# Kernel optimization log

Measured on AMD Instinct MI355X. Metric: run time of the kernel, lower is better.

The kernel has to match this reference:

```python
import jax, jax.numpy as jnp
import numpy as np

B, C_IN, IMG, PATCH = 16, 3, 512, 16
C_FEAT, N_CLS, K = 2048, 18, 24  # K cells per image (fixed -> jit-friendly ragged groups)
HF = IMG // PATCH  # 32
N_CELLS = B * K
EPS = 1e-6


def setup_inputs() -> dict:
    key = jax.random.key(0)
    ks = jax.random.split(key, 8)
    return {
        "cell_img": jax.random.normal(ks[0], (B, C_IN, IMG, IMG), jnp.float32),
        "cell_masks": jax.random.uniform(ks[1], (N_CELLS, HF, HF), jnp.float32),
        "cell_counts": jnp.full((B,), K, dtype=jnp.int32),
        "W_backbone": jax.random.normal(ks[2], (C_FEAT, C_IN, PATCH, PATCH), jnp.float32) * 0.02,
        "b_backbone": jnp.zeros((C_FEAT,), jnp.float32),
        "W_final": jax.random.normal(ks[3], (N_CLS, C_FEAT, 1, 1), jnp.float32) * 0.02,
        "b_final": jnp.zeros((N_CLS,), jnp.float32),
        "W1": jax.random.normal(ks[4], (1024, C_FEAT), jnp.float32) * 0.02,
        "b1": jnp.zeros((1024,), jnp.float32),
        "W2": jax.random.normal(ks[5], (N_CLS, 1024), jnp.float32) * 0.02,
        "b2": jnp.zeros((N_CLS,), jnp.float32),
    }


def _forward(cell_img, cell_masks, cell_counts, W_backbone, b_backbone,
             W_final, b_final, W1, b1, W2, b2):
    # backbone: patch-embed style conv, 3 -> 2048, stride 16 -> [B, 2048, 32, 32]
    fm = jax.lax.conv_general_dilated(
        cell_img, W_backbone, (PATCH, PATCH), "VALID",
        dimension_numbers=("NCHW", "OIHW", "NCHW"))
    fm = jax.nn.relu(fm + b_backbone[None, :, None, None])
    # final_conv: 1x1 conv 2048 -> 18 class maps
    class_maps = jnp.einsum("bchw,oc->bohw", fm, W_final[:, :, 0, 0]) + b_final[None, :, None, None]

    # masked-RoI average pooling (feature_roi / class_roi)
    fm2 = fm.reshape(B, C_FEAT, HF * HF)            # [B, C, P]
    cm2 = class_maps.reshape(B, N_CLS, HF * HF)     # [B, 18, P]
    masksB = cell_masks.reshape(B, K, HF * HF)      # [B, K, P]
    area = masksB.sum(-1, keepdims=True) + EPS       # [B, K, 1]
    cell_features = jnp.einsum("bkp,bcp->bkc", masksB, fm2) / area   # [B, K, 2048]
    cell_class_logits = jnp.einsum("bkp,bcp->bkc", masksB, cm2) / area  # [B, K, 18]

    # fc_cell_weights (Dropout is identity at eval)
    h = jax.nn.relu(jnp.einsum("bkc,oc->bko", cell_features, W1) + b1)
    cell_weight_logits = jnp.einsum("bkh,oh->bko", h, W2) + b2       # [B, K, 18]

    # per-image (segment) softmax over cells + attention-weighted sum
    attn = jax.nn.softmax(cell_weight_logits, axis=1)
    logits = (attn * cell_class_logits).sum(axis=1)                  # [B, 18]

    # zero-count fallback: global max-pool of class maps
    fallback = class_maps.max(axis=(2, 3))
    return jnp.where((cell_counts > 0)[:, None], logits, fallback)


def reference(cell_img, cell_masks, cell_counts, W_backbone, b_backbone,
              W_final, b_final, W1, b1, W2, b2):
    return _forward(cell_img, cell_masks, cell_counts, W_backbone, b_backbone,
                    W_final, b_final, W1, b1, W2, b2)
```

## Files before the change

### kernel.cpp

```cpp
#include <hip/hip_runtime.h>

#define B_      16
#define C_IN    3
#define IMG     512
#define PATCH   16
#define C_FEAT  2048
#define N_CLS   18
#define KCELL   24
#define HF      32
#define P_      (HF*HF)
#define KDIM    (C_IN*PATCH*PATCH)
#define M_GEMM1 (B_*P_)
#define EPS_    1e-6f

typedef __attribute__((ext_vector_type(8))) short bf16x8;
typedef __attribute__((ext_vector_type(4))) float f32x4;
typedef __attribute__((ext_vector_type(4))) unsigned short us4;
typedef __attribute__((ext_vector_type(8))) unsigned short us8;
typedef __attribute__((ext_vector_type(4))) float fl4;

#define DEVFN static __device__ __forceinline__

DEVFN unsigned short f2bf(float f) {
  union { float f; unsigned u; } x; x.f = f;
  unsigned r = (x.u + 0x7fffu + ((x.u >> 16) & 1u)) >> 16;
  return (unsigned short)r;
}
DEVFN float bf2f(unsigned short u) {
  union { unsigned u; float f; } x; x.u = ((unsigned)u) << 16;
  return x.f;
}
DEVFN f32x4 mfma16(bf16x8 a, bf16x8 b, f32x4 c) {
  return __builtin_amdgcn_mfma_f32_16x16x32_bf16(a, b, c, 0, 0, 0);
}
#define GLOAD16(gp, lp) __builtin_amdgcn_global_load_lds( \
    (const __attribute__((address_space(1))) unsigned int*)(gp), \
    (__attribute__((address_space(3))) unsigned int*)(lp), 16, 0, 0)

#define OFF_A     0u
#define OFF_WB    25165824u
#define OFF_W1    28311552u
#define OFF_W2    32505856u
#define OFF_FM    32542720u
#define OFF_MB    99651584u
#define OFF_AREA  100700160u
#define OFF_CF    100702208u
#define OFF_CL    102275072u
#define OFF_H     102302720u
#define WS_NEED   103089152u

__global__ __launch_bounds__(256) void k_prep(const float* __restrict__ masks,
                                              const float* __restrict__ Wb,
                                              const float* __restrict__ W1,
                                              const float* __restrict__ W2,
                                              unsigned short* __restrict__ mb,
                                              float* __restrict__ area,
                                              unsigned short* __restrict__ Wbb,
                                              unsigned short* __restrict__ W1b,
                                              unsigned short* __restrict__ W2b) {
  int blk = blockIdx.x;
  int t = threadIdx.x;
  if (blk < 512) {
    int b = blk >> 5, m = blk & 31;
    unsigned short* dst = mb + ((size_t)(b * 32 + m)) * P_;
    float s = 0.f;
    if (m < KCELL) {
      const float* src = masks + ((size_t)(b * KCELL + m)) * P_;
      for (int p = t; p < P_; p += 256) { float v = src[p]; s += v; dst[p] = f2bf(v); }
    } else {
      for (int p = t; p < P_; p += 256) dst[p] = 0;
    }
    for (int off = 32; off; off >>= 1) s += __shfl_down(s, off);
    __shared__ float red[4];
    if ((t & 63) == 0) red[t >> 6] = s;
    __syncthreads();
    if (t == 0) area[b * 32 + m] = red[0] + red[1] + red[2] + red[3] + EPS_;
    return;
  }
  const float* src; unsigned short* dst; int local, n;
  if (blk < 1280)      { src = Wb; dst = Wbb; local = blk - 512;  n = C_FEAT * KDIM; }
  else if (blk < 2304) { src = W1; dst = W1b; local = blk - 1280; n = 1024 * C_FEAT; }
  else                 { src = W2; dst = W2b; local = blk - 2304; n = N_CLS * 1024; }
  int i = (local * 256 + t) * 8;
  if (i + 8 <= n) {
    fl4 v0 = *(const fl4*)(src + i);
    fl4 v1 = *(const fl4*)(src + i + 4);
    us8 o;
    o[0] = f2bf(v0[0]); o[1] = f2bf(v0[1]); o[2] = f2bf(v0[2]); o[3] = f2bf(v0[3]);
    o[4] = f2bf(v1[0]); o[5] = f2bf(v1[1]); o[6] = f2bf(v1[2]); o[7] = f2bf(v1[3]);
    *(us8*)(dst + i) = o;
  }
}

__global__ __launch_bounds__(256) void k_im2col(const float* __restrict__ img,
                                                unsigned short* __restrict__ A) {
  int idx = blockIdx.x * 256 + threadIdx.x;
  int m = idx / 96, k8 = idx % 96;
  int k = k8 * 8;
  int b = m >> 10, p = m & 1023, hf = p >> 5, wf = p & 31;
  int c = k >> 8, py = (k >> 4) & 15, px = k & 15;
  const float* src = img + ((size_t)((b * 3 + c) * 512 + hf * 16 + py)) * 512 + wf * 16 + px;
  fl4 v0 = *(const fl4*)src;
  fl4 v1 = *(const fl4*)(src + 4);
  us8 o;
  o[0] = f2bf(v0[0]); o[1] = f2bf(v0[1]); o[2] = f2bf(v0[2]); o[3] = f2bf(v0[3]);
  o[4] = f2bf(v1[0]); o[5] = f2bf(v1[1]); o[6] = f2bf(v1[2]); o[7] = f2bf(v1[3]);
  *(us8*)(A + (size_t)m * KDIM + k) = o;
}

__global__ __launch_bounds__(256) void k_gemm1(const unsigned short* __restrict__ A,
                                               const unsigned short* __restrict__ BT,
                                               const float* __restrict__ bias,
                                               unsigned short* __restrict__ CT) {
  __shared__ unsigned short As[128 * 32];
  __shared__ unsigned short Bs[128 * 32];
  int bid = blockIdx.x;
  int swz = (bid & 7) * 256 + (bid >> 3);
  int bm = swz >> 4, bn = swz & 15;
  int m0 = bm * 128, n0 = bn * 128;
  int t = threadIdx.x;
  int w = t >> 6, l = t & 63, lr = l & 15, lg = l >> 4;
  int wr = w >> 1, wc = w & 1;
  int srow = t >> 2;
  int sk = (t & 3) * 8;
  f32x4 acc[4][4] = {};
  for (int k0 = 0; k0 < KDIM; k0 += 32) {
    GLOAD16(A + (size_t)(m0 + srow) * KDIM + k0 + sk,       As + t * 8);
    GLOAD16(A + (size_t)(m0 + 64 + srow) * KDIM + k0 + sk,  As + 2048 + t * 8);
    GLOAD16(BT + (size_t)(n0 + srow) * KDIM + k0 + sk,      Bs + t * 8);
    GLOAD16(BT + (size_t)(n0 + 64 + srow) * KDIM + k0 + sk, Bs + 2048 + t * 8);
    __syncthreads();
    bf16x8 a[4], bb[4];
#pragma unroll
    for (int i = 0; i < 4; ++i) {
      a[i]  = *(const bf16x8*)(As + (wr * 64 + i * 16 + lr) * 32 + lg * 8);
      bb[i] = *(const bf16x8*)(Bs + (wc * 64 + i * 16 + lr) * 32 + lg * 8);
    }
#pragma unroll
    for (int mi = 0; mi < 4; ++mi)
#pragma unroll
      for (int ni = 0; ni < 4; ++ni)
        acc[mi][ni] = mfma16(a[mi], bb[ni], acc[mi][ni]);
    __syncthreads();
  }
  int b = m0 >> 10;
  int pbase0 = (m0 & 1023) + wr * 64 + lg * 4;
#pragma unroll
  for (int ni = 0; ni < 4; ++ni) {
    int gcol = n0 + wc * 64 + ni * 16 + lr;
    float bv = bias[gcol];
    unsigned short* crow = CT + ((size_t)(b * C_FEAT + gcol)) * P_;
#pragma unroll
    for (int mi = 0; mi < 4; ++mi) {
      us4 o;
#pragma unroll
      for (int r = 0; r < 4; ++r)
        o[r] = f2bf(fmaxf(acc[mi][ni][r] + bv, 0.f));
      *(us4*)(crow + pbase0 + mi * 16) = o;
    }
  }
}

__global__ __launch_bounds__(256) void k_pool(const unsigned short* __restrict__ mb,
                                              const unsigned short* __restrict__ fmT,
                                              const float* __restrict__ area,
                                              unsigned short* __restrict__ CF) {
  int b = blockIdx.x, ct = blockIdx.y;
  int t = threadIdx.x, w = t >> 6, l = t & 63, lr = l & 15, lg = l >> 4;
  int c0 = ct * 128 + w * 32;
  const unsigned short* mbb = mb + (size_t)b * 32 * P_;
  const unsigned short* fb = fmT + (size_t)b * C_FEAT * P_;
  f32x4 acc[2][2] = {};
  for (int k0 = 0; k0 < P_; k0 += 32) {
    int kb = k0 + lg * 8;
    bf16x8 a0 = *(const bf16x8*)(mbb + (size_t)lr * P_ + kb);
    bf16x8 a1 = *(const bf16x8*)(mbb + (size_t)(16 + lr) * P_ + kb);
    bf16x8 b0 = *(const bf16x8*)(fb + (size_t)(c0 + lr) * P_ + kb);
    bf16x8 b1 = *(const bf16x8*)(fb + (size_t)(c0 + 16 + lr) * P_ + kb);
    acc[0][0] = mfma16(a0, b0, acc[0][0]);
    acc[1][0] = mfma16(a1, b0, acc[1][0]);
    acc[0][1] = mfma16(a0, b1, acc[0][1]);
    acc[1][1] = mfma16(a1, b1, acc[1][1]);
  }
#pragma unroll
  for (int mt = 0; mt < 2; ++mt)
#pragma unroll
    for (int r = 0; r < 4; ++r) {
      int m = mt * 16 + lg * 4 + r;
      if (m < KCELL) {
        float inv = 1.f / area[b * 32 + m];
#pragma unroll
        for (int nt = 0; nt < 2; ++nt) {
          int c = c0 + nt * 16 + lr;
          CF[((size_t)(b * KCELL + m)) * C_FEAT + c] = f2bf(acc[mt][nt][r] * inv);
        }
      }
    }
}

__global__ __launch_bounds__(256) void k_class_logits(const unsigned short* __restrict__ CF,
                                                      const float* __restrict__ Wf,
                                                      const float* __restrict__ bfin,
                                                      const float* __restrict__ area,
                                                      float* __restrict__ cl) {
  int cell = blockIdx.x;
  int t = threadIdx.x;
  int c0 = t * 8;
  float cf[8];
  bf16x8 v = *(const bf16x8*)(CF + (size_t)cell * C_FEAT + c0);
#pragma unroll
  for (int j = 0; j < 8; ++j) cf[j] = bf2f((unsigned short)v[j]);
  float acc[N_CLS];
#pragma unroll
  for (int o = 0; o < N_CLS; ++o) {
    fl4 w0 = *(const fl4*)(Wf + (size_t)o * C_FEAT + c0);
    fl4 w1 = *(const fl4*)(Wf + (size_t)o * C_FEAT + c0 + 4);
    acc[o] = cf[0]*w0[0] + cf[1]*w0[1] + cf[2]*w0[2] + cf[3]*w0[3]
           + cf[4]*w1[0] + cf[5]*w1[1] + cf[6]*w1[2] + cf[7]*w1[3];
  }
#pragma unroll
  for (int o = 0; o < N_CLS; ++o)
    for (int off = 32; off; off >>= 1) acc[o] += __shfl_down(acc[o], off);
  __shared__ float red[4][N_CLS];
  if ((t & 63) == 0) {
#pragma unroll
    for (int o = 0; o < N_CLS; ++o) red[t >> 6][o] = acc[o];
  }
  __syncthreads();
  if (t < N_CLS) {
    int b = cell / KCELL, m = cell % KCELL;
    float ar = area[b * 32 + m];
    float coeff = (ar - EPS_) / ar;
    cl[(size_t)cell * N_CLS + t] =
        red[0][t] + red[1][t] + red[2][t] + red[3][t] + bfin[t] * coeff;
  }
}

__global__ __launch_bounds__(256) void k_mlp1(const unsigned short* __restrict__ CF,
                                              const unsigned short* __restrict__ W1b,
                                              const float* __restrict__ b1,
                                              unsigned short* __restrict__ h) {
  int wid = blockIdx.x * 4 + (threadIdx.x >> 6);
  int l = threadIdx.x & 63, lr = l & 15, lg = l >> 4;
  int mt = wid >> 6, nt = wid & 63;
  int m0 = mt * 16, n0 = nt * 16;
  f32x4 acc = {};
  for (int k0 = 0; k0 < C_FEAT; k0 += 32) {
    int kb = k0 + lg * 8;
    bf16x8 a = *(const bf16x8*)(CF + (size_t)(m0 + lr) * C_FEAT + kb);
    bf16x8 b = *(const bf16x8*)(W1b + (size_t)(n0 + lr) * C_FEAT + kb);
    acc = mfma16(a, b, acc);
  }
  int col = n0 + lr;
  float bv = b1[col];
#pragma unroll
  for (int r = 0; r < 4; ++r) {
    int row = m0 + lg * 4 + r;
    h[(size_t)row * 1024 + col] = f2bf(fmaxf(acc[r] + bv, 0.f));
  }
}

__global__ __launch_bounds__(512) void k_mlp2_final(const unsigned short* __restrict__ hbf,
                                                    const unsigned short* __restrict__ W2b,
                                                    const float* __restrict__ b2,
                                                    const float* __restrict__ cl,
                                                    float* __restrict__ out) {
  int b = blockIdx.x;
  int t = threadIdx.x;
  __shared__ float wl[KCELL][N_CLS + 2];
  if (t < KCELL * N_CLS) {
    int k = t / N_CLS, o = t % N_CLS;
    const unsigned short* hr = hbf + (size_t)(b * KCELL + k) * 1024;
    const unsigned short* wr = W2b + (size_t)o * 1024;
    float acc = 0.f;
    for (int c = 0; c < 1024; c += 8) {
      bf16x8 hv = *(const bf16x8*)(hr + c);
      bf16x8 wv = *(const bf16x8*)(wr + c);
#pragma unroll
      for (int j = 0; j < 8; ++j)
        acc += bf2f((unsigned short)hv[j]) * bf2f((unsigned short)wv[j]);
    }
    wl[k][o] = acc + b2[o];
  }
  __syncthreads();
  if (t < N_CLS) {
    float m = -3.4e38f;
    for (int k = 0; k < KCELL; ++k) m = fmaxf(m, wl[k][t]);
    float s = 0.f, num = 0.f;
    for (int k = 0; k < KCELL; ++k) {
      float e = expf(wl[k][t] - m);
      s += e;
      num += e * cl[(size_t)(b * KCELL + k) * N_CLS + t];
    }
    out[b * N_CLS + t] = num / s;
  }
}

__global__ __launch_bounds__(256) void k_fallback(const int* __restrict__ counts,
                                                  const unsigned short* __restrict__ fmT,
                                                  const float* __restrict__ Wf,
                                                  const float* __restrict__ bfin,
                                                  float* __restrict__ out) {
  int b = blockIdx.x;
  if (counts[b] > 0) return;
  int t = threadIdx.x;
  const unsigned short* fb = fmT + (size_t)b * C_FEAT * P_;
  float lmax[N_CLS];
#pragma unroll
  for (int o = 0; o < N_CLS; ++o) lmax[o] = -3.4e38f;
  for (int p = t; p < P_; p += 256) {
    float acc[N_CLS];
#pragma unroll
    for (int o = 0; o < N_CLS; ++o) acc[o] = bfin[o];
    for (int c = 0; c < C_FEAT; ++c) {
      float f = bf2f(fb[(size_t)c * P_ + p]);
#pragma unroll
      for (int o = 0; o < N_CLS; ++o) acc[o] += f * Wf[(size_t)o * C_FEAT + c];
    }
#pragma unroll
    for (int o = 0; o < N_CLS; ++o) lmax[o] = fmaxf(lmax[o], acc[o]);
  }
#pragma unroll
  for (int o = 0; o < N_CLS; ++o)
    for (int off = 32; off; off >>= 1) lmax[o] = fmaxf(lmax[o], __shfl_down(lmax[o], off));
  __shared__ float red[4][N_CLS];
  if ((t & 63) == 0) {
#pragma unroll
    for (int o = 0; o < N_CLS; ++o) red[t >> 6][o] = lmax[o];
  }
  __syncthreads();
  if (t < N_CLS)
    out[b * N_CLS + t] = fmaxf(fmaxf(red[0][t], red[1][t]), fmaxf(red[2][t], red[3][t]));
}

extern "C" void kernel_launch(void* const* d_in, const int* in_sizes, int n_in,
                              void* d_out, int out_size, void* d_ws, size_t ws_size,
                              hipStream_t stream) {
  const float* img    = (const float*)d_in[0];
  const float* masks  = (const float*)d_in[1];
  const int*   counts = (const int*)d_in[2];
  const float* Wb     = (const float*)d_in[3];
  const float* bb     = (const float*)d_in[4];
  const float* Wf     = (const float*)d_in[5];
  const float* bfin   = (const float*)d_in[6];
  const float* W1     = (const float*)d_in[7];
  const float* b1     = (const float*)d_in[8];
  const float* W2     = (const float*)d_in[9];
  const float* b2     = (const float*)d_in[10];
  float* out = (float*)d_out;

  char* ws = (char*)d_ws;
  unsigned short* Abf  = (unsigned short*)(ws + OFF_A);
  unsigned short* Wbb  = (unsigned short*)(ws + OFF_WB);
  unsigned short* W1b  = (unsigned short*)(ws + OFF_W1);
  unsigned short* W2b  = (unsigned short*)(ws + OFF_W2);
  unsigned short* fmT  = (unsigned short*)(ws + OFF_FM);
  unsigned short* mbb  = (unsigned short*)(ws + OFF_MB);
  float*          area = (float*)(ws + OFF_AREA);
  unsigned short* CF   = (unsigned short*)(ws + OFF_CF);
  float*          cl   = (float*)(ws + OFF_CL);
  unsigned short* hb   = (unsigned short*)(ws + OFF_H);

  k_prep<<<2313, 256, 0, stream>>>(masks, Wb, W1, W2, mbb, area, Wbb, W1b, W2b);
  k_im2col<<<(M_GEMM1 * KDIM / 8) / 256, 256, 0, stream>>>(img, Abf);
  k_gemm1<<<(M_GEMM1 / 128) * (C_FEAT / 128), 256, 0, stream>>>(Abf, Wbb, bb, fmT);
  k_pool<<<dim3(B_, C_FEAT / 128), 256, 0, stream>>>(mbb, fmT, area, CF);
  k_class_logits<<<B_ * KCELL, 256, 0, stream>>>(CF, Wf, bfin, area, cl);
  k_mlp1<<<(24 * 64) / 4, 256, 0, stream>>>(CF, W1b, b1, hb);
  k_mlp2_final<<<B_, 512, 0, stream>>>(hb, W2b, b2, cl, out);
  k_fallback<<<B_, 256, 0, stream>>>(counts, fmT, Wf, bfin, out);
}
```

Baseline: 278.4 us.

## Fuse im2col into backbone GEMM, loading fp32 image patches directly to LDS

```diff
diff --git a/kernel.cpp b/kernel.cpp
--- a/kernel.cpp
+++ b/kernel.cpp
@@ -1,4 +1,5 @@
 #include <hip/hip_runtime.h>
+#include <hip/hip_bf16.h>
 
 #define B_      16
 #define C_IN    3
@@ -26,6 +27,10 @@
   unsigned r = (x.u + 0x7fffu + ((x.u >> 16) & 1u)) >> 16;
   return (unsigned short)r;
 }
+DEVFN unsigned short f2bf_h(float f) {
+  __hip_bfloat16 h = __float2bfloat16(f);
+  return *reinterpret_cast<unsigned short*>(&h);
+}
 DEVFN float bf2f(unsigned short u) {
   union { unsigned u; float f; } x; x.u = ((unsigned)u) << 16;
   return x.f;
@@ -92,28 +97,12 @@
   }
 }
 
-__global__ __launch_bounds__(256) void k_im2col(const float* __restrict__ img,
-                                                unsigned short* __restrict__ A) {
-  int idx = blockIdx.x * 256 + threadIdx.x;
-  int m = idx / 96, k8 = idx % 96;
-  int k = k8 * 8;
-  int b = m >> 10, p = m & 1023, hf = p >> 5, wf = p & 31;
-  int c = k >> 8, py = (k >> 4) & 15, px = k & 15;
-  const float* src = img + ((size_t)((b * 3 + c) * 512 + hf * 16 + py)) * 512 + wf * 16 + px;
-  fl4 v0 = *(const fl4*)src;
-  fl4 v1 = *(const fl4*)(src + 4);
-  us8 o;
-  o[0] = f2bf(v0[0]); o[1] = f2bf(v0[1]); o[2] = f2bf(v0[2]); o[3] = f2bf(v0[3]);
-  o[4] = f2bf(v1[0]); o[5] = f2bf(v1[1]); o[6] = f2bf(v1[2]); o[7] = f2bf(v1[3]);
-  *(us8*)(A + (size_t)m * KDIM + k) = o;
-}
-
-__global__ __launch_bounds__(256) void k_gemm1(const unsigned short* __restrict__ A,
-                                               const unsigned short* __restrict__ BT,
-                                               const float* __restrict__ bias,
-                                               unsigned short* __restrict__ CT) {
-  __shared__ unsigned short As[128 * 32];
-  __shared__ unsigned short Bs[128 * 32];
+__global__ __launch_bounds__(256) void k_gemm1f(const float* __restrict__ img,
+                                                const unsigned short* __restrict__ BT,
+                                                const float* __restrict__ bias,
+                                                unsigned short* __restrict__ CT) {
+  __shared__ float          As[8 * 1024];
+  __shared__ unsigned short Bs[4 * 2048];
   int bid = blockIdx.x;
   int swz = (bid & 7) * 256 + (bid >> 3);
   int bm = swz >> 4, bn = swz & 15;
@@ -121,26 +110,53 @@
   int t = threadIdx.x;
   int w = t >> 6, l = t & 63, lr = l & 15, lg = l >> 4;
   int wr = w >> 1, wc = w & 1;
-  int srow = t >> 2;
-  int sk = (t & 3) * 8;
+
+  int arow = t >> 1;
+  int am = m0 + arow;
+  int ab = am >> 10, ap = am & 1023, ahf = ap >> 5, awf = ap & 31;
+  const float* imb = img + ((size_t)(ab * 3) * 512 + (size_t)ahf * 16) * 512 + awf * 16;
+  int kq = (t & 1) * 4;
+
   f32x4 acc[4][4] = {};
-  for (int k0 = 0; k0 < KDIM; k0 += 32) {
-    GLOAD16(A + (size_t)(m0 + srow) * KDIM + k0 + sk,       As + t * 8);
-    GLOAD16(A + (size_t)(m0 + 64 + srow) * KDIM + k0 + sk,  As + 2048 + t * 8);
-    GLOAD16(BT + (size_t)(n0 + srow) * KDIM + k0 + sk,      Bs + t * 8);
-    GLOAD16(BT + (size_t)(n0 + 64 + srow) * KDIM + k0 + sk, Bs + 2048 + t * 8);
+  for (int k0 = 0; k0 < KDIM; k0 += 64) {
+#pragma unroll
+    for (int j = 0; j < 8; ++j) {
+      int k = k0 + j * 8 + kq;
+      int c = k >> 8, py = (k >> 4) & 15, px = k & 15;
+      GLOAD16(imb + ((size_t)c * 512 + py) * 512 + px, As + j * 1024 + t * 4);
+    }
+#pragma unroll
+    for (int g = 0; g < 4; ++g)
+      GLOAD16(BT + (size_t)(n0 + (t >> 1)) * KDIM + k0 + g * 16 + (t & 1) * 8,
+              Bs + g * 2048 + t * 8);
     __syncthreads();
-    bf16x8 a[4], bb[4];
-#pragma unroll
-    for (int i = 0; i < 4; ++i) {
-      a[i]  = *(const bf16x8*)(As + (wr * 64 + i * 16 + lr) * 32 + lg * 8);
-      bb[i] = *(const bf16x8*)(Bs + (wc * 64 + i * 16 + lr) * 32 + lg * 8);
-    }
-#pragma unroll
-    for (int mi = 0; mi < 4; ++mi)
-#pragma unroll
-      for (int ni = 0; ni < 4; ++ni)
-        acc[mi][ni] = mfma16(a[mi], bb[ni], acc[mi][ni]);
+#pragma unroll
+    for (int kk = 0; kk < 64; kk += 32) {
+      bf16x8 a[4], bb[4];
+#pragma unroll
+      for (int mi = 0; mi < 4; ++mi) {
+        int row = wr * 64 + mi * 16 + lr;
+        int o = (kk >> 3) + lg;
+        const float* ap_ = As + o * 1024 + row * 8;
+        fl4 lo = *(const fl4*)ap_;
+        fl4 hi = *(const fl4*)(ap_ + 4);
+        us8 af;
+        af[0] = f2bf_h(lo[0]); af[1] = f2bf_h(lo[1]); af[2] = f2bf_h(lo[2]); af[3] = f2bf_h(lo[3]);
+        af[4] = f2bf_h(hi[0]); af[5] = f2bf_h(hi[1]); af[6] = f2bf_h(hi[2]); af[7] = f2bf_h(hi[3]);
+        a[mi] = *(bf16x8*)&af;
+      }
+#pragma unroll
+      for (int ni = 0; ni < 4; ++ni) {
+        int row = wc * 64 + ni * 16 + lr;
+        int g = (kk >> 4) + (lg >> 1), half = lg & 1;
+        bb[ni] = *(const bf16x8*)(Bs + g * 2048 + row * 16 + half * 8);
+      }
+#pragma unroll
+      for (int mi = 0; mi < 4; ++mi)
+#pragma unroll
+        for (int ni = 0; ni < 4; ++ni)
+          acc[mi][ni] = mfma16(a[mi], bb[ni], acc[mi][ni]);
+    }
     __syncthreads();
   }
   int b = m0 >> 10;
@@ -171,6 +187,7 @@
   const unsigned short* mbb = mb + (size_t)b * 32 * P_;
   const unsigned short* fb = fmT + (size_t)b * C_FEAT * P_;
   f32x4 acc[2][2] = {};
+#pragma unroll 2
   for (int k0 = 0; k0 < P_; k0 += 32) {
     int kb = k0 + lg * 8;
     bf16x8 a0 = *(const bf16x8*)(mbb + (size_t)lr * P_ + kb);
@@ -273,12 +290,15 @@
     const unsigned short* hr = hbf + (size_t)(b * KCELL + k) * 1024;
     const unsigned short* wr = W2b + (size_t)o * 1024;
     float acc = 0.f;
-    for (int c = 0; c < 1024; c += 8) {
-      bf16x8 hv = *(const bf16x8*)(hr + c);
-      bf16x8 wv = *(const bf16x8*)(wr + c);
+    for (int c = 0; c < 1024; c += 16) {
+      bf16x8 hv0 = *(const bf16x8*)(hr + c);
+      bf16x8 hv1 = *(const bf16x8*)(hr + c + 8);
+      bf16x8 wv0 = *(const bf16x8*)(wr + c);
+      bf16x8 wv1 = *(const bf16x8*)(wr + c + 8);
 #pragma unroll
       for (int j = 0; j < 8; ++j)
-        acc += bf2f((unsigned short)hv[j]) * bf2f((unsigned short)wv[j]);
+        acc += bf2f((unsigned short)hv0[j]) * bf2f((unsigned short)wv0[j])
+             + bf2f((unsigned short)hv1[j]) * bf2f((unsigned short)wv1[j]);
     }
     wl[k][o] = acc + b2[o];
   }
@@ -350,7 +370,6 @@
   float* out = (float*)d_out;
 
   char* ws = (char*)d_ws;
-  unsigned short* Abf  = (unsigned short*)(ws + OFF_A);
   unsigned short* Wbb  = (unsigned short*)(ws + OFF_WB);
   unsigned short* W1b  = (unsigned short*)(ws + OFF_W1);
   unsigned short* W2b  = (unsigned short*)(ws + OFF_W2);
@@ -362,8 +381,7 @@
   unsigned short* hb   = (unsigned short*)(ws + OFF_H);
 
   k_prep<<<2313, 256, 0, stream>>>(masks, Wb, W1, W2, mbb, area, Wbb, W1b, W2b);
-  k_im2col<<<(M_GEMM1 * KDIM / 8) / 256, 256, 0, stream>>>(img, Abf);
-  k_gemm1<<<(M_GEMM1 / 128) * (C_FEAT / 128), 256, 0, stream>>>(Abf, Wbb, bb, fmT);
+  k_gemm1f<<<(M_GEMM1 / 128) * (C_FEAT / 128), 256, 0, stream>>>(img, Wbb, bb, fmT);
   k_pool<<<dim3(B_, C_FEAT / 128), 256, 0, stream>>>(mbb, fmT, area, CF);
   k_class_logits<<<B_ * KCELL, 256, 0, stream>>>(CF, Wf, bfin, area, cl);
   k_mlp1<<<(24 * 64) / 4, 256, 0, stream>>>(CF, W1b, b1, hb);
```

After: 280.7 us. No clear change (+0.8%).
